# Kernel tuning notes

Hardware: AMD Instinct MI355X
Metric: run time of the kernel (lower is better)

The kernel has to match this reference:

```python
import jax, jax.numpy as jnp
import numpy as np

B, T, H = 16, 2048, 1024

def setup_inputs() -> dict:
    key = jax.random.key(0)
    k1, k2, k3, k4 = jax.random.split(key, 4)
    stdv = 1.0 / np.sqrt(H)
    return {
        "hidden": jax.random.normal(k1, (B, H), dtype=jnp.float32),
        "encoder_outputs": jax.random.normal(k2, (B, T, 2 * H), dtype=jnp.float32),
        "W": jax.random.normal(k3, (H, 3 * H), dtype=jnp.float32) * stdv,  # nn.Linear(3H, H) weight
        "b": jnp.zeros((H,), dtype=jnp.float32),
        "v": jax.random.normal(k4, (H,), dtype=jnp.float32) * stdv,
    }

def reference(hidden, encoder_outputs, W, b, v):
    # hidden: (B,H); encoder_outputs: (B,T,2H)
    Bsz, Tlen, _ = encoder_outputs.shape
    Hrep = jnp.broadcast_to(hidden[:, None, :], (Bsz, Tlen, hidden.shape[-1]))  # (B,T,H)
    cat = jnp.concatenate([Hrep, encoder_outputs], axis=2)                      # (B,T,3H)
    energy = jnp.tanh(jnp.einsum('btk,hk->bth', cat, W) + b)                    # (B,T,H)
    scores = jnp.einsum('bth,h->bt', energy, v)[:, None, :]                     # (B,1,T), == bmm(v, energy^T)
    return jax.nn.softmax(scores, axis=2)
```

## Files before the change

### kernel.cpp

```cpp
#include <hip/hip_runtime.h>
#include <cstdint>

#define B_SZ 16
#define T_SZ 2048
#define H_SZ 1024
#define K_SZ 2048
#define M_SZ (B_SZ * T_SZ)

#define BM 128
#define BN 128
#define BK 64
#define LDK 72
#define KTILES (K_SZ / BK)

typedef _Float16 half8_t __attribute__((ext_vector_type(8)));
typedef float float4_t __attribute__((ext_vector_type(4)));

__global__ __launch_bounds__(256) void hpart_kernel(
    const float* __restrict__ hidden, const float* __restrict__ W,
    const float* __restrict__ bias, float* __restrict__ hpart) {
    int wave = (blockIdx.x * 256 + threadIdx.x) >> 6;
    int lane = threadIdx.x & 63;
    int b = wave >> 10;
    int h = wave & 1023;
    const float* wrow = W + (size_t)h * 3072;
    const float* hrow = hidden + b * H_SZ;
    int k0 = lane * 16;
    float acc = 0.f;
#pragma unroll
    for (int j = 0; j < 4; ++j) {
        float4_t wv = *(const float4_t*)(wrow + k0 + j * 4);
        float4_t hv = *(const float4_t*)(hrow + k0 + j * 4);
        acc += wv[0] * hv[0] + wv[1] * hv[1] + wv[2] * hv[2] + wv[3] * hv[3];
    }
#pragma unroll
    for (int off = 32; off >= 1; off >>= 1) acc += __shfl_xor(acc, off, 64);
    if (lane == 0) hpart[b * H_SZ + h] = acc + bias[h];
}

__global__ __launch_bounds__(256, 2) void attn_gemm_kernel(
    const float* __restrict__ enc, const float* __restrict__ W,
    const float* __restrict__ hpart, const float* __restrict__ v,
    float* __restrict__ partial) {
    __shared__ _Float16 Af[BM * LDK];
    __shared__ _Float16 Bf[BN * LDK];
    __shared__ float hp_s[BN];
    __shared__ float v_s[BN];

    const int bidx = blockIdx.x;
    const int blockN = bidx & 7;
    const int blockM = bidx >> 3;
    const int tid = threadIdx.x;
    const int lane = tid & 63;
    const int w = tid >> 6;
    const int wm = w & 1, wn = w >> 1;
    const int m16 = lane & 15, quad = lane >> 4;

    const int n0 = blockN * BN;
    const int batch = blockM >> 4;

    if (tid < BN) {
        hp_s[tid] = hpart[batch * H_SZ + n0 + tid];
        v_s[tid] = v[n0 + tid];
    }

    float4_t acc[4][4];
#pragma unroll
    for (int i = 0; i < 4; ++i)
#pragma unroll
        for (int j = 0; j < 4; ++j) acc[i][j] = (float4_t){0.f, 0.f, 0.f, 0.f};

    const float* Abase = enc + (size_t)(blockM * BM) * K_SZ;
    const float* Bbase = W + (size_t)n0 * 3072 + H_SZ;

    for (int kt = 0; kt < KTILES; ++kt) {
        __syncthreads();
        const float* Asrc0 = Abase + kt * BK;
#pragma unroll
        for (int i = 0; i < 4; ++i) {
            int f8 = i * 256 + tid;
            int r = f8 >> 3, c8 = f8 & 7;
            const float* src = Asrc0 + (size_t)r * K_SZ + c8 * 8;
            float4_t lo = *(const float4_t*)(src);
            float4_t hi = *(const float4_t*)(src + 4);
            half8_t hv;
            hv[0] = (_Float16)lo[0]; hv[1] = (_Float16)lo[1];
            hv[2] = (_Float16)lo[2]; hv[3] = (_Float16)lo[3];
            hv[4] = (_Float16)hi[0]; hv[5] = (_Float16)hi[1];
            hv[6] = (_Float16)hi[2]; hv[7] = (_Float16)hi[3];
            *(half8_t*)&Af[r * LDK + c8 * 8] = hv;
        }
        const float* Bsrc0 = Bbase + kt * BK;
#pragma unroll
        for (int i = 0; i < 4; ++i) {
            int f8 = i * 256 + tid;
            int r = f8 >> 3, c8 = f8 & 7;
            const float* src = Bsrc0 + (size_t)r * 3072 + c8 * 8;
            float4_t lo = *(const float4_t*)(src);
            float4_t hi = *(const float4_t*)(src + 4);
            half8_t hv;
            hv[0] = (_Float16)lo[0]; hv[1] = (_Float16)lo[1];
            hv[2] = (_Float16)lo[2]; hv[3] = (_Float16)lo[3];
            hv[4] = (_Float16)hi[0]; hv[5] = (_Float16)hi[1];
            hv[6] = (_Float16)hi[2]; hv[7] = (_Float16)hi[3];
            *(half8_t*)&Bf[r * LDK + c8 * 8] = hv;
        }
        __syncthreads();
#pragma unroll
        for (int ks = 0; ks < 2; ++ks) {
            half8_t afrag[4], bfrag[4];
#pragma unroll
            for (int tm = 0; tm < 4; ++tm)
                afrag[tm] = *(const half8_t*)&Af[(wm * 64 + tm * 16 + m16) * LDK + ks * 32 + quad * 8];
#pragma unroll
            for (int tn = 0; tn < 4; ++tn)
                bfrag[tn] = *(const half8_t*)&Bf[(wn * 64 + tn * 16 + m16) * LDK + ks * 32 + quad * 8];
#pragma unroll
            for (int tm = 0; tm < 4; ++tm)
#pragma unroll
                for (int tn = 0; tn < 4; ++tn)
                    acc[tm][tn] = __builtin_amdgcn_mfma_f32_16x16x32_f16(
                        afrag[tm], bfrag[tn], acc[tm][tn], 0, 0, 0);
        }
    }

    const int slice = blockN * 2 + wn;
#pragma unroll
    for (int tm = 0; tm < 4; ++tm) {
        float s0 = 0.f, s1 = 0.f, s2 = 0.f, s3 = 0.f;
#pragma unroll
        for (int tn = 0; tn < 4; ++tn) {
            int nl = wn * 64 + tn * 16 + m16;
            float hpv = hp_s[nl];
            float vv = v_s[nl];
            s0 += tanhf(acc[tm][tn][0] + hpv) * vv;
            s1 += tanhf(acc[tm][tn][1] + hpv) * vv;
            s2 += tanhf(acc[tm][tn][2] + hpv) * vv;
            s3 += tanhf(acc[tm][tn][3] + hpv) * vv;
        }
#pragma unroll
        for (int off = 1; off < 16; off <<= 1) {
            s0 += __shfl_xor(s0, off, 64);
            s1 += __shfl_xor(s1, off, 64);
            s2 += __shfl_xor(s2, off, 64);
            s3 += __shfl_xor(s3, off, 64);
        }
        if (m16 == 0) {
            int gm = blockM * BM + wm * 64 + tm * 16 + quad * 4;
            float* dst = partial + (size_t)slice * M_SZ + gm;
            dst[0] = s0; dst[1] = s1; dst[2] = s2; dst[3] = s3;
        }
    }
}

__global__ __launch_bounds__(256) void softmax_kernel(
    const float* __restrict__ partial, float* __restrict__ out) {
    __shared__ float red[256];
    const int b = blockIdx.x;
    const int tid = threadIdx.x;
    float sc[8];
    float mymax = -1e30f;
#pragma unroll
    for (int i = 0; i < 8; ++i) {
        int t = i * 256 + tid;
        float s = 0.f;
#pragma unroll
        for (int sl = 0; sl < 16; ++sl) s += partial[(size_t)sl * M_SZ + b * T_SZ + t];
        sc[i] = s;
        mymax = fmaxf(mymax, s);
    }
    red[tid] = mymax;
    __syncthreads();
    for (int off = 128; off >= 1; off >>= 1) {
        if (tid < off) red[tid] = fmaxf(red[tid], red[tid + off]);
        __syncthreads();
    }
    float mx = red[0];
    __syncthreads();
    float mysum = 0.f;
#pragma unroll
    for (int i = 0; i < 8; ++i) {
        sc[i] = expf(sc[i] - mx);
        mysum += sc[i];
    }
    red[tid] = mysum;
    __syncthreads();
    for (int off = 128; off >= 1; off >>= 1) {
        if (tid < off) red[tid] += red[tid + off];
        __syncthreads();
    }
    float inv = 1.0f / red[0];
#pragma unroll
    for (int i = 0; i < 8; ++i) out[b * T_SZ + i * 256 + tid] = sc[i] * inv;
}

extern "C" void kernel_launch(void* const* d_in, const int* in_sizes, int n_in,
                              void* d_out, int out_size, void* d_ws, size_t ws_size,
                              hipStream_t stream) {
    const float* hidden = (const float*)d_in[0];
    const float* enc    = (const float*)d_in[1];
    const float* W      = (const float*)d_in[2];
    const float* bias   = (const float*)d_in[3];
    const float* v      = (const float*)d_in[4];
    float* out = (float*)d_out;

    float* hpart = (float*)d_ws;
    float* partial = (float*)d_ws + B_SZ * H_SZ;

    hipLaunchKernelGGL(hpart_kernel, dim3(4096), dim3(256), 0, stream,
                       hidden, W, bias, hpart);
    hipLaunchKernelGGL(attn_gemm_kernel, dim3(2048), dim3(256), 0, stream,
                       enc, W, hpart, v, partial);
    hipLaunchKernelGGL(softmax_kernel, dim3(B_SZ), dim3(256), 0, stream,
                       partial, out);
}
```

Measured before the change: 675.1 us.

## Pre-convert encoder outputs and weights to fp16, load tiles via global_load_lds

```diff
diff --git a/kernel.cpp b/kernel.cpp
--- a/kernel.cpp
+++ b/kernel.cpp
@@ -15,6 +15,40 @@
 
 typedef _Float16 half8_t __attribute__((ext_vector_type(8)));
 typedef float float4_t __attribute__((ext_vector_type(4)));
+
+__device__ __forceinline__ void glds16(const _Float16* g, _Float16* l) {
+    __builtin_amdgcn_global_load_lds(
+        (const __attribute__((address_space(1))) void*)g,
+        (__attribute__((address_space(3))) void*)l, 16, 0, 0);
+}
+
+__global__ __launch_bounds__(256) void cvt_enc_kernel(
+    const float* __restrict__ src, _Float16* __restrict__ dst) {
+    size_t i = ((size_t)blockIdx.x * 256 + threadIdx.x) * 8;
+    float4_t a = *(const float4_t*)(src + i);
+    float4_t b = *(const float4_t*)(src + i + 4);
+    half8_t h;
+    h[0] = (_Float16)a[0]; h[1] = (_Float16)a[1];
+    h[2] = (_Float16)a[2]; h[3] = (_Float16)a[3];
+    h[4] = (_Float16)b[0]; h[5] = (_Float16)b[1];
+    h[6] = (_Float16)b[2]; h[7] = (_Float16)b[3];
+    *(half8_t*)(dst + i) = h;
+}
+
+__global__ __launch_bounds__(256) void cvt_w2_kernel(
+    const float* __restrict__ W, _Float16* __restrict__ dst) {
+    int idx8 = blockIdx.x * 256 + threadIdx.x;
+    int n = idx8 >> 8, k8 = (idx8 & 255) * 8;
+    const float* src = W + (size_t)n * 3072 + H_SZ + k8;
+    float4_t a = *(const float4_t*)(src);
+    float4_t b = *(const float4_t*)(src + 4);
+    half8_t h;
+    h[0] = (_Float16)a[0]; h[1] = (_Float16)a[1];
+    h[2] = (_Float16)a[2]; h[3] = (_Float16)a[3];
+    h[4] = (_Float16)b[0]; h[5] = (_Float16)b[1];
+    h[6] = (_Float16)b[2]; h[7] = (_Float16)b[3];
+    *(half8_t*)(dst + (size_t)n * K_SZ + k8) = h;
+}
 
 __global__ __launch_bounds__(256) void hpart_kernel(
     const float* __restrict__ hidden, const float* __restrict__ W,
@@ -36,6 +70,106 @@
 #pragma unroll
     for (int off = 32; off >= 1; off >>= 1) acc += __shfl_xor(acc, off, 64);
     if (lane == 0) hpart[b * H_SZ + h] = acc + bias[h];
+}
+
+__global__ __launch_bounds__(256, 2) void attn_gemm16_kernel(
+    const _Float16* __restrict__ A, const _Float16* __restrict__ Bm,
+    const float* __restrict__ hpart, const float* __restrict__ v,
+    float* __restrict__ partial) {
+    __shared__ _Float16 Af[BM * BK];
+    __shared__ _Float16 Bf[BN * BK];
+    __shared__ float hp_s[BN];
+    __shared__ float v_s[BN];
+
+    const int bidx = blockIdx.x;
+    const int blockN = bidx & 7;
+    const int blockM = bidx >> 3;
+    const int tid = threadIdx.x;
+    const int lane = tid & 63;
+    const int w = tid >> 6;
+    const int wm = w & 1, wn = w >> 1;
+    const int m16 = lane & 15, quad = lane >> 4;
+
+    const int n0 = blockN * BN;
+    const int batch = blockM >> 4;
+
+    if (tid < BN) {
+        hp_s[tid] = hpart[batch * H_SZ + n0 + tid];
+        v_s[tid] = v[n0 + tid];
+    }
+
+    float4_t acc[4][4];
+#pragma unroll
+    for (int i = 0; i < 4; ++i)
+#pragma unroll
+        for (int j = 0; j < 4; ++j) acc[i][j] = (float4_t){0.f, 0.f, 0.f, 0.f};
+
+    const _Float16* Abase = A + (size_t)(blockM * BM) * K_SZ;
+    const _Float16* Bbase = Bm + (size_t)n0 * K_SZ;
+
+    const int r_s = tid >> 3;
+    const int c8_s = (tid & 7) * 8;
+
+    for (int kt = 0; kt < KTILES; ++kt) {
+        __syncthreads();
+        const _Float16* As = Abase + kt * BK;
+        const _Float16* Bs = Bbase + kt * BK;
+#pragma unroll
+        for (int i = 0; i < 4; ++i) {
+            int idx16 = i * 256 + tid;
+            glds16(As + (size_t)(r_s + i * 32) * K_SZ + c8_s, &Af[idx16 * 8]);
+        }
+#pragma unroll
+        for (int i = 0; i < 4; ++i) {
+            int idx16 = i * 256 + tid;
+            glds16(Bs + (size_t)(r_s + i * 32) * K_SZ + c8_s, &Bf[idx16 * 8]);
+        }
+        __syncthreads();
+#pragma unroll
+        for (int ks = 0; ks < 2; ++ks) {
+            half8_t afrag[4], bfrag[4];
+#pragma unroll
+            for (int tm = 0; tm < 4; ++tm)
+                afrag[tm] = *(const half8_t*)&Af[(wm * 64 + tm * 16 + m16) * BK + ks * 32 + quad * 8];
+#pragma unroll
+            for (int tn = 0; tn < 4; ++tn)
+                bfrag[tn] = *(const half8_t*)&Bf[(wn * 64 + tn * 16 + m16) * BK + ks * 32 + quad * 8];
+#pragma unroll
+            for (int tm = 0; tm < 4; ++tm)
+#pragma unroll
+                for (int tn = 0; tn < 4; ++tn)
+                    acc[tm][tn] = __builtin_amdgcn_mfma_f32_16x16x32_f16(
+                        afrag[tm], bfrag[tn], acc[tm][tn], 0, 0, 0);
+        }
+    }
+
+    const int slice = blockN * 2 + wn;
+#pragma unroll
+    for (int tm = 0; tm < 4; ++tm) {
+        float s0 = 0.f, s1 = 0.f, s2 = 0.f, s3 = 0.f;
+#pragma unroll
+        for (int tn = 0; tn < 4; ++tn) {
+            int nl = wn * 64 + tn * 16 + m16;
+            float hpv = hp_s[nl];
+            float vv = v_s[nl];
+            s0 += tanhf(acc[tm][tn][0] + hpv) * vv;
+            s1 += tanhf(acc[tm][tn][1] + hpv) * vv;
+            s2 += tanhf(acc[tm][tn][2] + hpv) * vv;
+            s3 += tanhf(acc[tm][tn][3] + hpv) * vv;
+        }
+#pragma unroll
+        for (int off = 1; off < 16; off <<= 1) {
+            s0 += __shfl_xor(s0, off, 64);
+            s1 += __shfl_xor(s1, off, 64);
+            s2 += __shfl_xor(s2, off, 64);
+            s3 += __shfl_xor(s3, off, 64);
+        }
+        if (m16 == 0) {
+            int gm = blockM * BM + wm * 64 + tm * 16 + quad * 4;
+            float* dst = partial + (size_t)slice * M_SZ + gm;
+            dst[0] = s0; dst[1] = s1; dst[2] = s2; dst[3] = s3;
+        }
+    }
 }
 
 __global__ __launch_bounds__(256, 2) void attn_gemm_kernel(
@@ -204,13 +338,23 @@
     const float* v      = (const float*)d_in[4];
     float* out = (float*)d_out;
 
-    float* hpart = (float*)d_ws;
-    float* partial = (float*)d_ws + B_SZ * H_SZ;
+    float* hpart   = (float*)d_ws;
+    float* partial = hpart + B_SZ * H_SZ;
+    _Float16* w2h  = (_Float16*)(partial + 16 * M_SZ);
+    _Float16* e16  = w2h + (size_t)H_SZ * K_SZ;
+    const size_t need = (size_t)((char*)(e16 + (size_t)M_SZ * K_SZ) - (char*)d_ws);
 
     hipLaunchKernelGGL(hpart_kernel, dim3(4096), dim3(256), 0, stream,
                        hidden, W, bias, hpart);
-    hipLaunchKernelGGL(attn_gemm_kernel, dim3(2048), dim3(256), 0, stream,
-                       enc, W, hpart, v, partial);
+    if (ws_size >= need) {
+        hipLaunchKernelGGL(cvt_enc_kernel, dim3(32768), dim3(256), 0, stream, enc, e16);
+        hipLaunchKernelGGL(cvt_w2_kernel, dim3(1024), dim3(256), 0, stream, W, w2h);
+        hipLaunchKernelGGL(attn_gemm16_kernel, dim3(2048), dim3(256), 0, stream,
+                           e16, w2h, hpart, v, partial);
+    } else {
+        hipLaunchKernelGGL(attn_gemm_kernel, dim3(2048), dim3(256), 0, stream,
+                           enc, W, hpart, v, partial);
+    }
     hipLaunchKernelGGL(softmax_kernel, dim3(B_SZ), dim3(256), 0, stream,
                        partial, out);
 }
```

New measurement: 571.1 us. -15.4%, faster.
